# Kernel tuning notes

Measured on AMD Instinct MI355X. Metric: run time of the kernel, lower is better.

The kernel has to match this reference:

```python
import jax, jax.numpy as jnp
import numpy as np

G, N, K, H, D = 16, 256, 128, 32, 768
NUM_ATOM_TYPES = 128
NUM_EDGE_TYPES = NUM_ATOM_TYPES * NUM_ATOM_TYPES  # 16384
T_STEPS = 1000


def setup_inputs() -> dict:
    key = jax.random.key(0)
    ks = jax.random.split(key, 12)
    return {
        "pos": jax.random.normal(ks[0], (G, N, 3), dtype=jnp.float32) * 3.0,
        "x": jax.random.randint(ks[1], (G, N, 1), 0, NUM_ATOM_TYPES, dtype=jnp.int32),
        "t": jax.random.randint(ks[2], (G,), 0, T_STEPS, dtype=jnp.int32),
        "means": jax.random.uniform(ks[3], (T_STEPS, K), jnp.float32, 0.0, 3.0),
        "stds": jax.random.uniform(ks[4], (T_STEPS, K), jnp.float32, 0.0, 3.0),
        "mul_w": jnp.ones((NUM_EDGE_TYPES, 1), jnp.float32),
        "bias_w": jnp.zeros((NUM_EDGE_TYPES, 1), jnp.float32),
        "w1": jax.random.normal(ks[5], (K, K), jnp.float32) / np.sqrt(K),
        "b1": jnp.zeros((K,), jnp.float32),
        "w2": jax.random.normal(ks[6], (K, H), jnp.float32) / np.sqrt(K),
        "b2": jnp.zeros((H,), jnp.float32),
        "we": jax.random.normal(ks[7], (K, D), jnp.float32) / np.sqrt(K),
        "be": jnp.zeros((D,), jnp.float32),
    }


def _forward(pos, x, t, means, stds, mul_w, bias_w, w1, b1, w2, b2, we, be):
    atoms = x[:, :, 0]  # [G, N]
    edge_types = atoms[:, :, None] * NUM_ATOM_TYPES + atoms[:, None, :]  # [G,N,N]
    pad = atoms == 0  # [G, N]
    pos = jnp.where(pad[..., None], 0.0, pos)
    # delta_pos[g,i,j] = pos[g,j] - pos[g,i]
    delta_pos = pos[:, None, :, :] - pos[:, :, None, :]  # [G,N,N,3]
    sq = jnp.sum(delta_pos * delta_pos, axis=-1)  # [G,N,N]
    dist = jnp.sqrt(jnp.where(sq > 0, sq, 1.0)) * (sq > 0)  # safe norm, grad-safe at 0
    delta_pos = delta_pos / (dist[..., None] + 1e-5)
    # Gaussian basis expansion
    mul = mul_w[edge_types]   # [G,N,N,1]
    bias = bias_w[edge_types]  # [G,N,N,1]
    xg = mul * dist[..., None] + bias  # [G,N,N,1] -> broadcasts to K
    mean = means[t][:, None, None, :]               # [G,1,1,K]
    std = jnp.abs(stds[t])[:, None, None, :] + 1e-5  # [G,1,1,K]
    a = (2.0 * 3.14159) ** 0.5
    z = (xg - mean) / std
    edge_feature = jnp.exp(-0.5 * z * z) / (a * std)  # [G,N,N,K]
    # NonLinear MLP -> attn bias per head
    h = jax.nn.gelu(edge_feature @ w1 + b1, approximate=False)
    attn_bias = h @ w2 + b2  # [G,N,N,H]
    attn_bias = jnp.transpose(attn_bias, (0, 3, 1, 2))  # [G,H,N,N]
    attn_bias = jnp.where(pad[:, None, None, :], -jnp.inf, attn_bias)
    # masked sum over source nodes + edge projection
    ef = jnp.where(pad[:, None, :, None], 0.0, edge_feature)
    sum_ef = jnp.sum(ef, axis=-2)  # [G,N,K]
    merge = sum_ef @ we + be  # [G,N,D]
    return dist, delta_pos, attn_bias, merge


def reference(pos, x, t, means, stds, mul_w, bias_w, w1, b1, w2, b2, we, be):
    return _forward(pos, x, t, means, stds, mul_w, bias_w, w1, b1, w2, b2, we, be)
```

## Files before the change

### kernel.cpp

```cpp
#include <hip/hip_runtime.h>
#include <hip/hip_bf16.h>
#include <math.h>

#define Gn 16
#define Nn 256
#define Kf 128
#define Hh 32
#define Dd 768
#define NEG_BIG (-3.0e38f)
#define INV_A 0.3989422804014327f
#define NHALF_LOG2E (-0.7213475204444817f)
#define GELU_C (-2.4554669f)

typedef __attribute__((ext_vector_type(8))) short bf16x8;
typedef __attribute__((ext_vector_type(4))) float f32x4;

static __device__ __forceinline__ float fast_exp2(float x) {
#if __has_builtin(__builtin_amdgcn_exp2f)
    return __builtin_amdgcn_exp2f(x);
#else
    return exp2f(x);
#endif
}
static __device__ __forceinline__ float fast_rcp(float x) {
#if __has_builtin(__builtin_amdgcn_rcpf)
    return __builtin_amdgcn_rcpf(x);
#else
    return 1.0f / x;
#endif
}

static __device__ __forceinline__ unsigned short f2bf(float f) {
    union { float f; unsigned int u; } v; v.f = f;
    unsigned int r = v.u + 0x7FFF + ((v.u >> 16) & 1);
    return (unsigned short)(r >> 16);
}

static __device__ __forceinline__ void load_lds16(const void* g, void* l) {
    __builtin_amdgcn_global_load_lds(
        (const __attribute__((address_space(1))) unsigned int*)g,
        (__attribute__((address_space(3))) unsigned int*)l, 16, 0, 0);
}

static __device__ __forceinline__ void stage8k(const char* gsrc, char* lbase,
                                               int wq, int lane) {
    const char* g0 = gsrc + wq * 1024 + lane * 16;
    char* l0 = lbase + wq * 1024 + lane * 16;
    load_lds16(g0, l0);
    load_lds16(g0 + 4096, l0 + 4096);
}

__global__ __launch_bounds__(256)
void prep_kernel(const float* __restrict__ w1, const float* __restrict__ w2,
                 const int* __restrict__ tarr, const float* __restrict__ means,
                 const float* __restrict__ stds,
                 char* __restrict__ w1c, char* __restrict__ w2s,
                 float4* __restrict__ coef)
{
    const int idx = blockIdx.x * 256 + threadIdx.x;
    if (idx < 2048) {
        const int ks = idx >> 9;
        const int n  = (idx >> 2) & 127;
        const int s  = idx & 3;
        unsigned short v[8];
#pragma unroll
        for (int e = 0; e < 8; ++e) {
            const int k = ks * 32 + s * 8 + e;
            v[e] = f2bf(w1[k * Kf + n]);
        }
        *(uint4*)(w1c + ks * 8192 + n * 64 + ((s ^ (n & 3)) << 4)) = *(const uint4*)v;
    } else if (idx < 2304) {
        const int e2 = idx - 2048;
        const int m = e2 >> 3, s2 = e2 & 7;
        unsigned short v[8];
#pragma unroll
        for (int e = 0; e < 8; ++e) {
            const int k = s2 * 8 + e;
            v[e] = f2bf(w2[k * Hh + m]);
        }
        *(uint4*)(w2s + m * 256 + ((s2 ^ (m & 7)) << 4)) = *(const uint4*)v;
    } else if (idx < 4352) {
        const int e3 = idx - 2304;
        const int g = e3 >> 7, k = e3 & 127;
        const int tg = tarr[g];
        const float mean = means[tg * Kf + k];
        const float sd   = fabsf(stds[tg * Kf + k]) + 1e-5f;
        const float inv  = 1.0f / sd;
        coef[g * Kf + k] =
            make_float4(mean, NHALF_LOG2E * inv * inv, log2f(inv * INV_A), 0.f);
    }
}

__global__ __launch_bounds__(256, 3)
void graph3d_attn_kernel(const float* __restrict__ pos,
                         const int* __restrict__ atoms,
                         const float* __restrict__ mul_w,
                         const float* __restrict__ bias_w,
                         const float* __restrict__ b1,
                         const float* __restrict__ b2,
                         const char* __restrict__ w1c,
                         const char* __restrict__ w2s,
                         const float4* __restrict__ coef,
                         float* __restrict__ ws_sum,
                         float* __restrict__ out_dist,
                         float* __restrict__ out_delta,
                         float* __restrict__ out_attn)
{
    const int tid  = threadIdx.x;
    const int half = blockIdx.x;
    const int i    = blockIdx.y;
    const int g    = blockIdx.z;
    const int j0   = half * 128;

    __shared__ __align__(16) unsigned short s_tile[128 * 128];
    __shared__ __align__(16) unsigned short s_chunk[4096];
    __shared__ float2 s_xgm[128];
    __shared__ __align__(16) float s_b1[128];
    __shared__ float  s_b2[32];
    __shared__ __align__(8) float s_mean[128];
    __shared__ __align__(8) float s_Ak[128];
    __shared__ __align__(8) float s_Ck[128];
    __shared__ __align__(8) float s_part[4][128];

    const int lane = tid & 63, wq = tid >> 6;
    const int l15 = lane & 15, lhi = lane >> 4;

    const int ai = atoms[g * Nn + i];
    float pix = pos[(g * Nn + i) * 3 + 0];
    float piy = pos[(g * Nn + i) * 3 + 1];
    float piz = pos[(g * Nn + i) * 3 + 2];
    if (ai == 0) { pix = 0.f; piy = 0.f; piz = 0.f; }

    if (tid < 128) {
        const float4 c = coef[g * Kf + tid];
        s_mean[tid] = c.x; s_Ak[tid] = c.y; s_Ck[tid] = c.z;
        s_b1[tid]   = b1[tid];

        const int j  = j0 + tid;
        const int aj = atoms[g * Nn + j];
        float pjx = pos[(g * Nn + j) * 3 + 0];
        float pjy = pos[(g * Nn + j) * 3 + 1];
        float pjz = pos[(g * Nn + j) * 3 + 2];
        if (aj == 0) { pjx = 0.f; pjy = 0.f; pjz = 0.f; }
        const float dx = pjx - pix, dy = pjy - piy, dz = pjz - piz;
        const float sq = dx * dx + dy * dy + dz * dz;
        const float dist = (sq > 0.f) ? sqrtf(sq) : 0.f;
        const float inv_d = 1.f / (dist + 1e-5f);
        const size_t base = (size_t)(g * Nn + i) * Nn + j;
        out_dist[base] = dist;
        out_delta[base * 3 + 0] = dx * inv_d;
        out_delta[base * 3 + 1] = dy * inv_d;
        out_delta[base * 3 + 2] = dz * inv_d;
        const int et = ai * 128 + aj;
        const float xg = fmaf(mul_w[et], dist, bias_w[et]);
        s_xgm[tid] = make_float2(xg, (aj == 0) ? 0.f : 1.f);
    } else if (tid < 160) {
        s_b2[tid - 128] = b2[tid - 128];
    }
    __syncthreads();

    stage8k(w1c, (char*)s_chunk, wq, lane);

    {
        const int k2 = tid & 63;
        const int jq = tid >> 6;
        const float2 mn = *(const float2*)&s_mean[2 * k2];
        const float2 Ak = *(const float2*)&s_Ak[2 * k2];
        const float2 Ck = *(const float2*)&s_Ck[2 * k2];
        float psum0 = 0.f, psum1 = 0.f;
        const int jb = jq * 32;
        const int colb = 4 * k2;
#pragma unroll 8
        for (int j = jb; j < jb + 32; ++j) {
            const float2 xm = s_xgm[j];
            const float d0 = xm.x - mn.x;
            const float d1 = xm.x - mn.y;
            const float e0 = fast_exp2(fmaf(Ak.x, d0 * d0, Ck.x));
            const float e1 = fast_exp2(fmaf(Ak.y, d1 * d1, Ck.y));
            psum0 = fmaf(e0, xm.y, psum0);
            psum1 = fmaf(e1, xm.y, psum1);
            const __hip_bfloat162 p = __float22bfloat162_rn(make_float2(e0, e1));
            *(unsigned int*)((char*)s_tile + j * 256 + (colb ^ ((j & 7) << 4))) =
                *(const unsigned int*)&p;
        }
        *(float2*)&s_part[jq][2 * k2] = make_float2(psum0, psum1);
    }
    __syncthreads();
    if (tid < 128) {
        ws_sum[((size_t)(g * Nn + i) * 2 + half) * Kf + tid] =
            (s_part[0][tid] + s_part[1][tid]) + (s_part[2][tid] + s_part[3][tid]);
    }

    const int jrow0 = wq * 32 + l15;
    const int jrow1 = jrow0 + 16;
    const int aslot = (lhi ^ (l15 & 3)) << 4;

    f32x4 acc[8][2];
#pragma unroll
    for (int a = 0; a < 8; ++a)
#pragma unroll
        for (int b = 0; b < 2; ++b) acc[a][b] = (f32x4){0.f, 0.f, 0.f, 0.f};

#pragma unroll
    for (int ks = 0; ks < 4; ++ks) {
        if (ks) __syncthreads();
        const int kb = ks * 64 + lhi * 16;
        const bf16x8 b0 = *(const bf16x8*)((char*)s_tile + jrow0 * 256 + (kb ^ ((jrow0 & 7) << 4)));
        const bf16x8 b1f = *(const bf16x8*)((char*)s_tile + jrow1 * 256 + (kb ^ ((jrow1 & 7) << 4)));
        bf16x8 a[8];
#pragma unroll
        for (int nf = 0; nf < 8; ++nf)
            a[nf] = *(const bf16x8*)((char*)s_chunk + (nf * 16 + l15) * 64 + aslot);
        __syncthreads();
        if (ks < 3) stage8k(w1c + (ks + 1) * 8192, (char*)s_chunk, wq, lane);
        else        stage8k(w2s, (char*)s_chunk, wq, lane);
#pragma unroll
        for (int nf = 0; nf < 8; ++nf) {
            acc[nf][0] = __builtin_amdgcn_mfma_f32_16x16x32_bf16(a[nf], b0, acc[nf][0], 0, 0, 0);
            acc[nf][1] = __builtin_amdgcn_mfma_f32_16x16x32_bf16(a[nf], b1f, acc[nf][1], 0, 0, 0);
        }
    }

#pragma unroll
    for (int nf = 0; nf < 8; ++nf) {
        const float4 bb = *(const float4*)&s_b1[nf * 16 + lhi * 4];
        const int colb = 32 * nf + 8 * lhi;
#pragma unroll
        for (int jf = 0; jf < 2; ++jf) {
            const int j = wq * 32 + jf * 16 + l15;
            float h[4];
#pragma unroll
            for (int r = 0; r < 4; ++r) {
                const float v = acc[nf][jf][r] + ((const float*)&bb)[r];
                const float sg = fast_rcp(1.0f + fast_exp2(GELU_C * v));
                h[r] = v * sg;
            }
            const __hip_bfloat162 p0 = __float22bfloat162_rn(make_float2(h[0], h[1]));
            const __hip_bfloat162 p1 = __float22bfloat162_rn(make_float2(h[2], h[3]));
            uint2 u;
            u.x = *(const unsigned int*)&p0;
            u.y = *(const unsigned int*)&p1;
            *(uint2*)((char*)s_tile + j * 256 + (colb ^ ((j & 7) << 4))) = u;
        }
    }
    __syncthreads();

    f32x4 acc2[2][2];
#pragma unroll
    for (int a = 0; a < 2; ++a)
#pragma unroll
        for (int b = 0; b < 2; ++b) acc2[a][b] = (f32x4){0.f, 0.f, 0.f, 0.f};

#pragma unroll
    for (int ks = 0; ks < 4; ++ks) {
        const int kb = ks * 64 + lhi * 16;
        const bf16x8 bh0 = *(const bf16x8*)((char*)s_tile + jrow0 * 256 + (kb ^ ((jrow0 & 7) << 4)));
        const bf16x8 bh1 = *(const bf16x8*)((char*)s_tile + jrow1 * 256 + (kb ^ ((jrow1 & 7) << 4)));
#pragma unroll
        for (int mf = 0; mf < 2; ++mf) {
            const int m = mf * 16 + l15;
            const bf16x8 a2 = *(const bf16x8*)((char*)s_chunk + m * 256 + (kb ^ ((m & 7) << 4)));
            acc2[mf][0] = __builtin_amdgcn_mfma_f32_16x16x32_bf16(a2, bh0, acc2[mf][0], 0, 0, 0);
            acc2[mf][1] = __builtin_amdgcn_mfma_f32_16x16x32_bf16(a2, bh1, acc2[mf][1], 0, 0, 0);
        }
    }

    const size_t attn_g = (size_t)g * Hh * (Nn * Nn) + (size_t)i * Nn + j0;
#pragma unroll
    for (int mf = 0; mf < 2; ++mf) {
#pragma unroll
        for (int jf = 0; jf < 2; ++jf) {
            const int jloc = wq * 32 + jf * 16 + l15;
            const float keep = s_xgm[jloc].y;
#pragma unroll
            for (int r = 0; r < 4; ++r) {
                const int m = mf * 16 + lhi * 4 + r;
                float v = acc2[mf][jf][r] + s_b2[m];
                if (keep == 0.f) v = NEG_BIG;
                out_attn[attn_g + (size_t)m * (Nn * Nn) + jloc] = v;
            }
        }
    }
}

__global__ __launch_bounds__(256)
void graph3d_merge_kernel(const float* __restrict__ ws_sum,
                          const float* __restrict__ we,
                          const float* __restrict__ be,
                          float* __restrict__ out_merge)
{
    const int tid = threadIdx.x;
    const int r0  = blockIdx.x * 16;
    __shared__ __align__(16) float s_rows[16][128];

#pragma unroll
    for (int p = 0; p < 8; ++p) {
        const int e = p * 256 + tid;
        const int r = e >> 7, k = e & 127;
        const size_t gi = (size_t)(r0 + r);
        s_rows[r][k] = ws_sum[(gi * 2 + 0) * Kf + k] + ws_sum[(gi * 2 + 1) * Kf + k];
    }
    __syncthreads();

    float acc[16][3];
#pragma unroll
    for (int r = 0; r < 16; ++r) { acc[r][0] = 0.f; acc[r][1] = 0.f; acc[r][2] = 0.f; }

    for (int k4 = 0; k4 < 32; ++k4) {
        const int k = k4 * 4;
        float w[4][3];
#pragma unroll
        for (int q = 0; q < 4; ++q) {
            w[q][0] = we[(k + q) * Dd + tid];
            w[q][1] = we[(k + q) * Dd + tid + 256];
            w[q][2] = we[(k + q) * Dd + tid + 512];
        }
#pragma unroll
        for (int r = 0; r < 16; ++r) {
            const float4 s = ((const float4*)&s_rows[r][0])[k4];
#pragma unroll
            for (int c = 0; c < 3; ++c) {
                acc[r][c] = fmaf(s.x, w[0][c], acc[r][c]);
                acc[r][c] = fmaf(s.y, w[1][c], acc[r][c]);
                acc[r][c] = fmaf(s.z, w[2][c], acc[r][c]);
                acc[r][c] = fmaf(s.w, w[3][c], acc[r][c]);
            }
        }
    }

    const float be0 = be[tid], be1 = be[tid + 256], be2 = be[tid + 512];
#pragma unroll
    for (int r = 0; r < 16; ++r) {
        const size_t ob = (size_t)(r0 + r) * Dd;
        out_merge[ob + tid]       = acc[r][0] + be0;
        out_merge[ob + tid + 256] = acc[r][1] + be1;
        out_merge[ob + tid + 512] = acc[r][2] + be2;
    }
}

extern "C" void kernel_launch(void* const* d_in, const int* in_sizes, int n_in,
                              void* d_out, int out_size, void* d_ws, size_t ws_size,
                              hipStream_t stream) {
    const float* pos    = (const float*)d_in[0];
    const int*   x      = (const int*)  d_in[1];
    const int*   t      = (const int*)  d_in[2];
    const float* means  = (const float*)d_in[3];
    const float* stds   = (const float*)d_in[4];
    const float* mul_w  = (const float*)d_in[5];
    const float* bias_w = (const float*)d_in[6];
    const float* w1     = (const float*)d_in[7];
    const float* b1     = (const float*)d_in[8];
    const float* w2     = (const float*)d_in[9];
    const float* b2     = (const float*)d_in[10];
    const float* we     = (const float*)d_in[11];
    const float* be     = (const float*)d_in[12];

    float* out = (float*)d_out;
    float* out_dist  = out;
    float* out_delta = out + (size_t)Gn * Nn * Nn;
    float* out_attn  = out + (size_t)Gn * Nn * Nn * 4;
    float* out_merge = out + (size_t)Gn * Nn * Nn * 4 + (size_t)Gn * Hh * Nn * Nn;

    float* ws_sum = (float*)d_ws;
    char*  w1c  = (char*)d_ws + (size_t)Gn * Nn * 2 * Kf * 4;
    char*  w2s  = w1c + 4 * 8192;
    float4* coef = (float4*)(w2s + 8192);

    prep_kernel<<<17, 256, 0, stream>>>(w1, w2, t, means, stds, w1c, w2s, coef);

    dim3 gridA(2, Nn, Gn);
    graph3d_attn_kernel<<<gridA, 256, 0, stream>>>(
        pos, x, mul_w, bias_w, b1, b2, w1c, w2s, coef,
        ws_sum, out_dist, out_delta, out_attn);

    graph3d_merge_kernel<<<(Gn * Nn) / 16, 256, 0, stream>>>(
        ws_sum, we, be, out_merge);
}
```

Baseline: 135.6 us.

## Replace per-edge shared staging with register shuffles and ballots, raise occupancy

The attention kernel no longer stages per-edge distances, masks, biases, Gaussian coefficients or partial sums in shared memory. Every wave now computes xg for two edges and broadcasts it with shuffles, builds the pad mask with ballots, and reduces the K-sums with xor shuffles before writing them straight to the workspace. This removes one barrier and several LDS arrays, and launch bounds go from 3 to 4 blocks per CU. The W1/W2 LDS swizzle layouts change, the W2 staging prep is widened to 16 slots per row, and the merge kernel is split over a second grid dimension for more parallelism. In exchange, each thread does redundant distance math, and register pressure under the tighter bound may cause spills.

Result: faster. 131.7 us (-2.9%).

```diff
diff --git a/kernel.cpp b/kernel.cpp
--- a/kernel.cpp
+++ b/kernel.cpp
@@ -68,10 +68,11 @@
             const int k = ks * 32 + s * 8 + e;
             v[e] = f2bf(w1[k * Kf + n]);
         }
-        *(uint4*)(w1c + ks * 8192 + n * 64 + ((s ^ (n & 3)) << 4)) = *(const uint4*)v;
-    } else if (idx < 2304) {
+        *(uint4*)(w1c + ks * 8192 + n * 64 + ((s ^ ((n >> 1) & 3)) << 4)) =
+            *(const uint4*)v;
+    } else if (idx < 2560) {
         const int e2 = idx - 2048;
-        const int m = e2 >> 3, s2 = e2 & 7;
+        const int m = e2 >> 4, s2 = e2 & 15;
         unsigned short v[8];
 #pragma unroll
         for (int e = 0; e < 8; ++e) {
@@ -79,8 +80,8 @@
             v[e] = f2bf(w2[k * Hh + m]);
         }
         *(uint4*)(w2s + m * 256 + ((s2 ^ (m & 7)) << 4)) = *(const uint4*)v;
-    } else if (idx < 4352) {
-        const int e3 = idx - 2304;
+    } else if (idx < 4608) {
+        const int e3 = idx - 2560;
         const int g = e3 >> 7, k = e3 & 127;
         const int tg = tarr[g];
         const float mean = means[tg * Kf + k];
@@ -91,7 +92,7 @@
     }
 }
 
-__global__ __launch_bounds__(256, 3)
+__global__ __launch_bounds__(256, 4)
 void graph3d_attn_kernel(const float* __restrict__ pos,
                          const int* __restrict__ atoms,
                          const float* __restrict__ mul_w,
@@ -114,13 +115,6 @@
 
     __shared__ __align__(16) unsigned short s_tile[128 * 128];
     __shared__ __align__(16) unsigned short s_chunk[4096];
-    __shared__ float2 s_xgm[128];
-    __shared__ __align__(16) float s_b1[128];
-    __shared__ float  s_b2[32];
-    __shared__ __align__(8) float s_mean[128];
-    __shared__ __align__(8) float s_Ak[128];
-    __shared__ __align__(8) float s_Ck[128];
-    __shared__ __align__(8) float s_part[4][128];
 
     const int lane = tid & 63, wq = tid >> 6;
     const int l15 = lane & 15, lhi = lane >> 4;
@@ -131,69 +125,93 @@
     float piz = pos[(g * Nn + i) * 3 + 2];
     if (ai == 0) { pix = 0.f; piy = 0.f; piz = 0.f; }
 
-    if (tid < 128) {
-        const float4 c = coef[g * Kf + tid];
-        s_mean[tid] = c.x; s_Ak[tid] = c.y; s_Ck[tid] = c.z;
-        s_b1[tid]   = b1[tid];
-
-        const int j  = j0 + tid;
-        const int aj = atoms[g * Nn + j];
-        float pjx = pos[(g * Nn + j) * 3 + 0];
-        float pjy = pos[(g * Nn + j) * 3 + 1];
-        float pjz = pos[(g * Nn + j) * 3 + 2];
-        if (aj == 0) { pjx = 0.f; pjy = 0.f; pjz = 0.f; }
-        const float dx = pjx - pix, dy = pjy - piy, dz = pjz - piz;
-        const float sq = dx * dx + dy * dy + dz * dz;
-        const float dist = (sq > 0.f) ? sqrtf(sq) : 0.f;
-        const float inv_d = 1.f / (dist + 1e-5f);
-        const size_t base = (size_t)(g * Nn + i) * Nn + j;
-        out_dist[base] = dist;
-        out_delta[base * 3 + 0] = dx * inv_d;
-        out_delta[base * 3 + 1] = dy * inv_d;
-        out_delta[base * 3 + 2] = dz * inv_d;
-        const int et = ai * 128 + aj;
-        const float xg = fmaf(mul_w[et], dist, bias_w[et]);
-        s_xgm[tid] = make_float2(xg, (aj == 0) ? 0.f : 1.f);
-    } else if (tid < 160) {
-        s_b2[tid - 128] = b2[tid - 128];
+    const int jA = lane, jB = lane + 64;
+    const int aA = atoms[g * Nn + j0 + jA];
+    const int aB = atoms[g * Nn + j0 + jB];
+    float pax = pos[(g * Nn + j0 + jA) * 3 + 0];
+    float pay = pos[(g * Nn + j0 + jA) * 3 + 1];
+    float paz = pos[(g * Nn + j0 + jA) * 3 + 2];
+    if (aA == 0) { pax = 0.f; pay = 0.f; paz = 0.f; }
+    float pbx = pos[(g * Nn + j0 + jB) * 3 + 0];
+    float pby = pos[(g * Nn + j0 + jB) * 3 + 1];
+    float pbz = pos[(g * Nn + j0 + jB) * 3 + 2];
+    if (aB == 0) { pbx = 0.f; pby = 0.f; pbz = 0.f; }
+
+    const float dxA = pax - pix, dyA = pay - piy, dzA = paz - piz;
+    const float sqA = dxA * dxA + dyA * dyA + dzA * dzA;
+    const float dA  = (sqA > 0.f) ? sqrtf(sqA) : 0.f;
+    const float ivA = 1.f / (dA + 1e-5f);
+    const int  etA  = ai * 128 + aA;
+    const float xgA = fmaf(mul_w[etA], dA, bias_w[etA]);
+
+    const float dxB = pbx - pix, dyB = pby - piy, dzB = pbz - piz;
+    const float sqB = dxB * dxB + dyB * dyB + dzB * dzB;
+    const float dB  = (sqB > 0.f) ? sqrtf(sqB) : 0.f;
+    const float ivB = 1.f / (dB + 1e-5f);
+    const int  etB  = ai * 128 + aB;
+    const float xgB = fmaf(mul_w[etB], dB, bias_w[etB]);
+
+    const unsigned long long mA = __ballot(aA != 0);
+    const unsigned long long mB = __ballot(aB != 0);
+
+    if (wq == (lane >> 5)) {
+        const size_t base = (size_t)(g * Nn + i) * Nn + j0 + jA;
+        out_dist[base] = dA;
+        out_delta[base * 3 + 0] = dxA * ivA;
+        out_delta[base * 3 + 1] = dyA * ivA;
+        out_delta[base * 3 + 2] = dzA * ivA;
+    } else if (wq == 2 + (lane >> 5)) {
+        const size_t base = (size_t)(g * Nn + i) * Nn + j0 + jB;
+        out_dist[base] = dB;
+        out_delta[base * 3 + 0] = dxB * ivB;
+        out_delta[base * 3 + 1] = dyB * ivB;
+        out_delta[base * 3 + 2] = dzB * ivB;
+    }
+
+    stage8k(w1c, (char*)s_chunk, wq, lane);
+
+    {
+        const int kpl = lane >> 2, jsub = lane & 3;
+        const int kp  = wq * 16 + kpl;
+        const float4 c0 = coef[g * Kf + 2 * kp];
+        const float4 c1 = coef[g * Kf + 2 * kp + 1];
+        const float xsrc = (jsub & 2) ? xgB : xgA;
+        const unsigned long long msel = (jsub & 2) ? mB : mA;
+        const unsigned int mm = (jsub & 1) ? (unsigned int)(msel >> 32)
+                                           : (unsigned int)msel;
+        const int sbase = (jsub & 1) * 32;
+        char* rowb = (char*)s_tile + jsub * 32 * 256;
+        unsigned int wa[8];
+#pragma unroll
+        for (int s = 0; s < 8; ++s) wa[s] = (unsigned int)(4 * kp) ^ (unsigned int)(s << 4);
+
+        float ps0 = 0.f, ps1 = 0.f;
+#pragma unroll
+        for (int jj = 0; jj < 32; ++jj) {
+            const float xgj = __shfl(xsrc, sbase + jj);
+            const float kf  = (float)((mm >> jj) & 1u);
+            const float d0 = xgj - c0.x;
+            const float d1 = xgj - c1.x;
+            const float e0 = fast_exp2(fmaf(c0.y, d0 * d0, c0.z));
+            const float e1 = fast_exp2(fmaf(c1.y, d1 * d1, c1.z));
+            ps0 = fmaf(e0, kf, ps0);
+            ps1 = fmaf(e1, kf, ps1);
+            const __hip_bfloat162 p = __float22bfloat162_rn(make_float2(e0, e1));
+            *(unsigned int*)(rowb + jj * 256 + wa[jj & 7]) = *(const unsigned int*)&p;
+        }
+        ps0 += __shfl_xor(ps0, 1); ps0 += __shfl_xor(ps0, 2);
+        ps1 += __shfl_xor(ps1, 1); ps1 += __shfl_xor(ps1, 2);
+        if (jsub == 0)
+            *(float2*)&ws_sum[((size_t)(g * Nn + i) * 2 + half) * Kf + 2 * kp] =
+                make_float2(ps0, ps1);
     }
     __syncthreads();
 
-    stage8k(w1c, (char*)s_chunk, wq, lane);
-
-    {
-        const int k2 = tid & 63;
-        const int jq = tid >> 6;
-        const float2 mn = *(const float2*)&s_mean[2 * k2];
-        const float2 Ak = *(const float2*)&s_Ak[2 * k2];
-        const float2 Ck = *(const float2*)&s_Ck[2 * k2];
-        float psum0 = 0.f, psum1 = 0.f;
-        const int jb = jq * 32;
-        const int colb = 4 * k2;
-#pragma unroll 8
-        for (int j = jb; j < jb + 32; ++j) {
-            const float2 xm = s_xgm[j];
-            const float d0 = xm.x - mn.x;
-            const float d1 = xm.x - mn.y;
-            const float e0 = fast_exp2(fmaf(Ak.x, d0 * d0, Ck.x));
-            const float e1 = fast_exp2(fmaf(Ak.y, d1 * d1, Ck.y));
-            psum0 = fmaf(e0, xm.y, psum0);
-            psum1 = fmaf(e1, xm.y, psum1);
-            const __hip_bfloat162 p = __float22bfloat162_rn(make_float2(e0, e1));
-            *(unsigned int*)((char*)s_tile + j * 256 + (colb ^ ((j & 7) << 4))) =
-                *(const unsigned int*)&p;
-        }
-        *(float2*)&s_part[jq][2 * k2] = make_float2(psum0, psum1);
-    }
-    __syncthreads();
-    if (tid < 128) {
-        ws_sum[((size_t)(g * Nn + i) * 2 + half) * Kf + tid] =
-            (s_part[0][tid] + s_part[1][tid]) + (s_part[2][tid] + s_part[3][tid]);
-    }
-
-    const int jrow0 = wq * 32 + l15;
-    const int jrow1 = jrow0 + 16;
-    const int aslot = (lhi ^ (l15 & 3)) << 4;
+    const int jrow0 = wq * 32 + l15, jrow1 = jrow0 + 16;
+    const char* tb0 = (const char*)s_tile + jrow0 * 256;
+    const char* tb1 = (const char*)s_tile + jrow1 * 256;
+    const int sw0 = (jrow0 & 7) << 4, sw1 = (jrow1 & 7) << 4;
+    const int aoff = l15 * 64 + ((lhi ^ ((l15 >> 1) & 3)) << 4);
 
     f32x4 acc[8][2];
 #pragma unroll
@@ -205,29 +223,30 @@
     for (int ks = 0; ks < 4; ++ks) {
         if (ks) __syncthreads();
         const int kb = ks * 64 + lhi * 16;
-        const bf16x8 b0 = *(const bf16x8*)((char*)s_tile + jrow0 * 256 + (kb ^ ((jrow0 & 7) << 4)));
-        const bf16x8 b1f = *(const bf16x8*)((char*)s_tile + jrow1 * 256 + (kb ^ ((jrow1 & 7) << 4)));
+        const bf16x8 b0  = *(const bf16x8*)(tb0 + (kb ^ sw0));
+        const bf16x8 b1f = *(const bf16x8*)(tb1 + (kb ^ sw1));
         bf16x8 a[8];
 #pragma unroll
         for (int nf = 0; nf < 8; ++nf)
-            a[nf] = *(const bf16x8*)((char*)s_chunk + (nf * 16 + l15) * 64 + aslot);
+            a[nf] = *(const bf16x8*)((const char*)s_chunk + nf * 1024 + aoff);
         __syncthreads();
         if (ks < 3) stage8k(w1c + (ks + 1) * 8192, (char*)s_chunk, wq, lane);
         else        stage8k(w2s, (char*)s_chunk, wq, lane);
 #pragma unroll
         for (int nf = 0; nf < 8; ++nf) {
-            acc[nf][0] = __builtin_amdgcn_mfma_f32_16x16x32_bf16(a[nf], b0, acc[nf][0], 0, 0, 0);
+            acc[nf][0] = __builtin_amdgcn_mfma_f32_16x16x32_bf16(a[nf], b0,  acc[nf][0], 0, 0, 0);
             acc[nf][1] = __builtin_amdgcn_mfma_f32_16x16x32_bf16(a[nf], b1f, acc[nf][1], 0, 0, 0);
         }
     }
 
 #pragma unroll
     for (int nf = 0; nf < 8; ++nf) {
-        const float4 bb = *(const float4*)&s_b1[nf * 16 + lhi * 4];
+        const float4 bb = *(const float4*)(b1 + nf * 16 + lhi * 4);
         const int colb = 32 * nf + 8 * lhi;
 #pragma unroll
         for (int jf = 0; jf < 2; ++jf) {
-            const int j = wq * 32 + jf * 16 + l15;
+            const char* tb = jf ? tb1 : tb0;
+            const int sw = jf ? sw1 : sw0;
             float h[4];
 #pragma unroll
             for (int r = 0; r < 4; ++r) {
@@ -240,7 +259,7 @@
             uint2 u;
             u.x = *(const unsigned int*)&p0;
             u.y = *(const unsigned int*)&p1;
-            *(uint2*)((char*)s_tile + j * 256 + (colb ^ ((j & 7) << 4))) = u;
+            *(uint2*)(const_cast<char*>(tb) + (colb ^ sw)) = u;
         }
     }
     __syncthreads();
@@ -254,29 +273,32 @@
 #pragma unroll
     for (int ks = 0; ks < 4; ++ks) {
         const int kb = ks * 64 + lhi * 16;
-        const bf16x8 bh0 = *(const bf16x8*)((char*)s_tile + jrow0 * 256 + (kb ^ ((jrow0 & 7) << 4)));
-        const bf16x8 bh1 = *(const bf16x8*)((char*)s_tile + jrow1 * 256 + (kb ^ ((jrow1 & 7) << 4)));
+        const bf16x8 bh0 = *(const bf16x8*)(tb0 + (kb ^ sw0));
+        const bf16x8 bh1 = *(const bf16x8*)(tb1 + (kb ^ sw1));
 #pragma unroll
         for (int mf = 0; mf < 2; ++mf) {
             const int m = mf * 16 + l15;
-            const bf16x8 a2 = *(const bf16x8*)((char*)s_chunk + m * 256 + (kb ^ ((m & 7) << 4)));
+            const bf16x8 a2 = *(const bf16x8*)((const char*)s_chunk + m * 256 + (kb ^ ((m & 7) << 4)));
             acc2[mf][0] = __builtin_amdgcn_mfma_f32_16x16x32_bf16(a2, bh0, acc2[mf][0], 0, 0, 0);
             acc2[mf][1] = __builtin_amdgcn_mfma_f32_16x16x32_bf16(a2, bh1, acc2[mf][1], 0, 0, 0);
         }
     }
 
     const size_t attn_g = (size_t)g * Hh * (Nn * Nn) + (size_t)i * Nn + j0;
-#pragma unroll
-    for (int mf = 0; mf < 2; ++mf) {
-#pragma unroll
-        for (int jf = 0; jf < 2; ++jf) {
-            const int jloc = wq * 32 + jf * 16 + l15;
-            const float keep = s_xgm[jloc].y;
+    const unsigned long long mOwn = (wq & 2) ? mB : mA;
+#pragma unroll
+    for (int jf = 0; jf < 2; ++jf) {
+        const int jloc = wq * 32 + jf * 16 + l15;
+        const int bit  = (wq & 1) * 32 + jf * 16 + l15;
+        const bool keep = (mOwn >> bit) & 1ull;
+#pragma unroll
+        for (int mf = 0; mf < 2; ++mf) {
+            const float4 b2v = *(const float4*)(b2 + mf * 16 + lhi * 4);
 #pragma unroll
             for (int r = 0; r < 4; ++r) {
                 const int m = mf * 16 + lhi * 4 + r;
-                float v = acc2[mf][jf][r] + s_b2[m];
-                if (keep == 0.f) v = NEG_BIG;
+                float v = acc2[mf][jf][r] + ((const float*)&b2v)[r];
+                if (!keep) v = NEG_BIG;
                 out_attn[attn_g + (size_t)m * (Nn * Nn) + jloc] = v;
             }
         }
@@ -290,7 +312,8 @@
                           float* __restrict__ out_merge)
 {
     const int tid = threadIdx.x;
-    const int r0  = blockIdx.x * 16;
+    const int bd  = blockIdx.x;
+    const int r0  = blockIdx.y * 16;
     __shared__ __align__(16) float s_rows[16][128];
 
 #pragma unroll
@@ -302,40 +325,31 @@
     }
     __syncthreads();
 
-    float acc[16][3];
-#pragma unroll
-    for (int r = 0; r < 16; ++r) { acc[r][0] = 0.f; acc[r][1] = 0.f; acc[r][2] = 0.f; }
+    const int col = bd * 256 + tid;
+    float acc[16];
+#pragma unroll
+    for (int r = 0; r < 16; ++r) acc[r] = 0.f;
 
     for (int k4 = 0; k4 < 32; ++k4) {
         const int k = k4 * 4;
-        float w[4][3];
-#pragma unroll
-        for (int q = 0; q < 4; ++q) {
-            w[q][0] = we[(k + q) * Dd + tid];
-            w[q][1] = we[(k + q) * Dd + tid + 256];
-            w[q][2] = we[(k + q) * Dd + tid + 512];
-        }
+        const float w0 = we[(k + 0) * Dd + col];
+        const float w1v = we[(k + 1) * Dd + col];
+        const float w2v = we[(k + 2) * Dd + col];
+        const float w3 = we[(k + 3) * Dd + col];
 #pragma unroll
         for (int r = 0; r < 16; ++r) {
             const float4 s = ((const float4*)&s_rows[r][0])[k4];
-#pragma unroll
-            for (int c = 0; c < 3; ++c) {
-                acc[r][c] = fmaf(s.x, w[0][c], acc[r][c]);
-                acc[r][c] = fmaf(s.y, w[1][c], acc[r][c]);
-                acc[r][c] = fmaf(s.z, w[2][c], acc[r][c]);
-                acc[r][c] = fmaf(s.w, w[3][c], acc[r][c]);
-            }
-        }
-    }
-
-    const float be0 = be[tid], be1 = be[tid + 256], be2 = be[tid + 512];
-#pragma unroll
-    for (int r = 0; r < 16; ++r) {
-        const size_t ob = (size_t)(r0 + r) * Dd;
-        out_merge[ob + tid]       = acc[r][0] + be0;
-        out_merge[ob + tid + 256] = acc[r][1] + be1;
-        out_merge[ob + tid + 512] = acc[r][2] + be2;
-    }
+            acc[r] = fmaf(s.x, w0, acc[r]);
+            acc[r] = fmaf(s.y, w1v, acc[r]);
+            acc[r] = fmaf(s.z, w2v, acc[r]);
+            acc[r] = fmaf(s.w, w3, acc[r]);
+        }
+    }
+
+    const float b = be[col];
+#pragma unroll
+    for (int r = 0; r < 16; ++r)
+        out_merge[(size_t)(r0 + r) * Dd + col] = acc[r] + b;
 }
 
 extern "C" void kernel_launch(void* const* d_in, const int* in_sizes, int n_in,
@@ -366,13 +380,14 @@
     char*  w2s  = w1c + 4 * 8192;
     float4* coef = (float4*)(w2s + 8192);
 
-    prep_kernel<<<17, 256, 0, stream>>>(w1, w2, t, means, stds, w1c, w2s, coef);
+    prep_kernel<<<18, 256, 0, stream>>>(w1, w2, t, means, stds, w1c, w2s, coef);
 
     dim3 gridA(2, Nn, Gn);
     graph3d_attn_kernel<<<gridA, 256, 0, stream>>>(
         pos, x, mul_w, bias_w, b1, b2, w1c, w2s, coef,
         ws_sum, out_dist, out_delta, out_attn);
 
-    graph3d_merge_kernel<<<(Gn * Nn) / 16, 256, 0, stream>>>(
+    dim3 gridB(3, 256);
+    graph3d_merge_kernel<<<gridB, 256, 0, stream>>>(
         ws_sum, we, be, out_merge);
 }
```
